# Optimization experiments

Hardware: AMD Instinct MI355X
Metric: run time of the kernel (lower is better)

Reference implementation:

```python
import jax, jax.numpy as jnp
import numpy as np

B, L, D, H = 4, 2048, 1024, 16
DK = D // H  # 64


def setup_inputs() -> dict:
    key = jax.random.key(0)
    ks = jax.random.split(key, 5)
    x = jax.random.normal(ks[0], (B, L, D), dtype=jnp.float32)
    scale = 1.0 / np.sqrt(D)
    W_qkv = jax.random.normal(ks[1], (D, 3 * D), dtype=jnp.float32) * scale
    b_qkv = jnp.zeros((3 * D,), dtype=jnp.float32)
    W_out = jax.random.normal(ks[2], (D, D), dtype=jnp.float32) * scale
    b_out = jnp.zeros((D,), dtype=jnp.float32)
    return {"x": x, "W_qkv": W_qkv, "b_qkv": b_qkv, "W_out": W_out, "b_out": b_out}


def reference(x, W_qkv, b_qkv, W_out, b_out):
    Bx, Lx, Dx = x.shape
    qkv = x @ W_qkv + b_qkv                      # [B, L, 3D]
    q, k, v = jnp.split(qkv, 3, axis=-1)
    # [B, H, L, d_k]
    q = q.reshape(Bx, Lx, H, DK).transpose(0, 2, 1, 3)
    k = k.reshape(Bx, Lx, H, DK).transpose(0, 2, 1, 3)
    v = v.reshape(Bx, Lx, H, DK).transpose(0, 2, 1, 3)
    scores = jnp.einsum('bhqd,bhkd->bhqk', q, k) / np.sqrt(DK)
    causal = jnp.tril(jnp.ones((Lx, Lx), dtype=bool))
    scores = jnp.where(causal[None, None], scores, -jnp.inf)
    attn = jax.nn.softmax(scores, axis=-1)       # [B, H, L, L]
    out = jnp.einsum('bhqk,bhkd->bhqd', attn, v)
    out = out.transpose(0, 2, 1, 3).reshape(Bx, Lx, Dx)
    return out @ W_out + b_out
```

## Files before the change

### kernel.cpp

```cpp
#include <hip/hip_runtime.h>
#include <stdint.h>

#define B_ 4
#define L_ 2048
#define D_ 1024
#define H_ 16
#define DK_ 64

typedef __attribute__((ext_vector_type(8))) short bf16x8;
typedef __attribute__((ext_vector_type(4))) float f32x4;
typedef unsigned short bfu;

#define MFMA(a, b, c) __builtin_amdgcn_mfma_f32_16x16x32_bf16((a), (b), (c), 0, 0, 0)

__device__ __forceinline__ unsigned short f2bf(float f) {
  union { float f; unsigned int u; } v; v.f = f;
  unsigned int u = v.u;
  return (unsigned short)((u + 0x7fffu + ((u >> 16) & 1u)) >> 16);
}

__device__ __forceinline__ void gll16(const void* g, void* l) {
  __builtin_amdgcn_global_load_lds(
      (const __attribute__((address_space(1))) void*)g,
      (__attribute__((address_space(3))) void*)l, 16, 0, 0);
}


__global__ __launch_bounds__(256) void cast_x(const float* __restrict__ in,
                                              bfu* __restrict__ out, int n4) {
  int i = blockIdx.x * 256 + threadIdx.x;
  if (i >= n4) return;
  float4 v = ((const float4*)in)[i];
  ushort4 o;
  o.x = f2bf(v.x); o.y = f2bf(v.y); o.z = f2bf(v.z); o.w = f2bf(v.w);
  ((ushort4*)out)[i] = o;
}

__global__ void transpose_cast(const float* __restrict__ in, bfu* __restrict__ out,
                               int R, int C) {
  __shared__ float tile[32][33];
  int c0 = blockIdx.x * 32, r0 = blockIdx.y * 32;
  int tx = threadIdx.x, ty = threadIdx.y;
#pragma unroll
  for (int i = ty; i < 32; i += 8)
    tile[i][tx] = in[(size_t)(r0 + i) * C + c0 + tx];
  __syncthreads();
#pragma unroll
  for (int i = ty; i < 32; i += 8)
    out[(size_t)(c0 + i) * R + r0 + tx] = f2bf(tile[tx][i]);
}


template <int EPI>
__global__ __launch_bounds__(256, 3) void gemm_bt(
    const bfu* __restrict__ A, const bfu* __restrict__ Bt,
    const float* __restrict__ bias, bfu* __restrict__ Qg, bfu* __restrict__ Kg,
    bfu* __restrict__ Vtg, float* __restrict__ Out, int M, int N, int K) {
  __shared__ __align__(16) bfu As[128 * 64];
  __shared__ __align__(16) bfu Bs[128 * 64];
  const int tid = threadIdx.x;
  const int lane = tid & 63;
  const int w = tid >> 6;
  const int wr = w >> 1, wc = w & 1;
  const int m0 = blockIdx.y * 128;
  const int n0 = blockIdx.x * 128;
  const int l15 = lane & 15, l4 = lane >> 4;

  f32x4 acc[4][4] = {};

  for (int k0 = 0; k0 < K; k0 += 64) {
    __syncthreads();
#pragma unroll
    for (int i = 0; i < 4; ++i) {
      int lb = i * 256 + tid;
      int r = lb >> 3;
      int c16p = lb & 7;
      int c16 = c16p ^ (r & 7);
      gll16(A + (size_t)(m0 + r) * K + k0 + c16 * 8, (char*)As + (size_t)lb * 16);
      gll16(Bt + (size_t)(n0 + r) * K + k0 + c16 * 8, (char*)Bs + (size_t)lb * 16);
    }
    __syncthreads();
#pragma unroll
    for (int kk = 0; kk < 2; ++kk) {
      bf16x8 af[4], bfr[4];
#pragma unroll
      for (int mi = 0; mi < 4; ++mi) {
        int r = wr * 64 + mi * 16 + l15;
        int c16 = (kk * 4 + l4) ^ (r & 7);
        af[mi] = *(const bf16x8*)((const char*)As + (size_t)r * 128 + c16 * 16);
      }
#pragma unroll
      for (int ni = 0; ni < 4; ++ni) {
        int r = wc * 64 + ni * 16 + l15;
        int c16 = (kk * 4 + l4) ^ (r & 7);
        bfr[ni] = *(const bf16x8*)((const char*)Bs + (size_t)r * 128 + c16 * 16);
      }
#pragma unroll
      for (int mi = 0; mi < 4; ++mi)
#pragma unroll
        for (int ni = 0; ni < 4; ++ni)
          acc[mi][ni] = MFMA(af[mi], bfr[ni], acc[mi][ni]);
    }
  }

#pragma unroll
  for (int ni = 0; ni < 4; ++ni) {
    int gn = n0 + wc * 64 + ni * 16 + l15;
    float bv = bias[gn];
    if (EPI == 0) {
      int sec = gn >> 10;
      int rem = gn & 1023;
      int hh = rem >> 6, dk = rem & 63;
#pragma unroll
      for (int mi = 0; mi < 4; ++mi) {
#pragma unroll
        for (int rg = 0; rg < 4; ++rg) {
          int gm = m0 + wr * 64 + mi * 16 + l4 * 4 + rg;
          int bb = gm >> 11, ll = gm & 2047;
          float v = acc[mi][ni][rg] + bv;
          size_t hd = (size_t)(bb * H_ + hh);
          if (sec == 0)
            Qg[(hd * L_ + ll) * DK_ + dk] = f2bf(v * 0.18033688011112042f);
          else if (sec == 1)
            Kg[(hd * L_ + ll) * DK_ + dk] = f2bf(v);
          else {
            int kv = ll & 63;
            int s = (kv & 32) | (((kv >> 2) & 3) << 3) | (((kv >> 4) & 1) << 2) | (kv & 3);
            Vtg[(hd * DK_ + dk) * L_ + ((ll & ~63) | s)] = f2bf(v);
          }
        }
      }
    } else {
#pragma unroll
      for (int mi = 0; mi < 4; ++mi)
#pragma unroll
        for (int rg = 0; rg < 4; ++rg) {
          int gm = m0 + wr * 64 + mi * 16 + l4 * 4 + rg;
          Out[(size_t)gm * 1024 + gn] = acc[mi][ni][rg] + bv;
        }
    }
  }
}


__global__ __launch_bounds__(256, 4) void attn(const bfu* __restrict__ Qg,
                                               const bfu* __restrict__ Kg,
                                               const bfu* __restrict__ Vtg,
                                               bfu* __restrict__ Ao) {
  __shared__ __align__(16) bfu Ks[2 * 64 * 64];
  __shared__ __align__(16) bfu Vs[2 * 64 * 64];
  __shared__ __align__(16) bfu Qs[64 * 64];

  const int tid = threadIdx.x;
  const int lane = tid & 63;
  const int w = tid >> 6;
  const int l15 = lane & 15, l4 = lane >> 4;

  const int hid = blockIdx.x;
  const int xcd = hid & 7, slot = hid >> 3;
  const int bh = (xcd << 3) | (slot >> 4);
  const int xq = slot & 15;
  const int b = bh >> 4, h = bh & 15;

  for (int seg = 0; seg < 2; ++seg) {
    const int qb = (seg == 0) ? xq : 31 - xq;
    const int q0 = qb * 64;
    const int nt = qb + 1;

#pragma unroll
    for (int i = 0; i < 2; ++i) {
      int lb = i * 256 + tid;
      int r = lb >> 3, c16 = (lb & 7) ^ (r & 7);
      gll16(Qg + ((size_t)bh * L_ + q0 + r) * DK_ + c16 * 8, (char*)Qs + lb * 16);
      gll16(Kg + ((size_t)bh * L_ + r) * DK_ + c16 * 8, (char*)Ks + lb * 16);
      gll16(Vtg + ((size_t)bh * DK_ + r) * L_ + c16 * 8, (char*)Vs + lb * 16);
    }
    asm volatile("s_waitcnt vmcnt(0)" ::: "memory");
    asm volatile("s_barrier" ::: "memory");

    bf16x8 qf[2];
#pragma unroll
    for (int kk = 0; kk < 2; ++kk) {
      int r = w * 16 + l15;
      int c16 = (kk * 4 + l4) ^ (r & 7);
      qf[kk] = *(const bf16x8*)((const char*)Qs + r * 128 + c16 * 16);
    }

    f32x4 acco[4] = {};
    float m = -1e30f, l = 0.f;

    for (int t = 0; t < nt; ++t) {
      const int cur = t & 1;
      const char* Kc = (const char*)Ks + cur * 8192;
      const char* Vc = (const char*)Vs + cur * 8192;

      if (t + 1 < nt) {
        const int nb = (t + 1) & 1, nkv = (t + 1) * 64;
#pragma unroll
        for (int i = 0; i < 2; ++i) {
          int lb = i * 256 + tid;
          int r = lb >> 3, c16 = (lb & 7) ^ (r & 7);
          gll16(Kg + ((size_t)bh * L_ + nkv + r) * DK_ + c16 * 8,
                (char*)Ks + nb * 8192 + lb * 16);
          gll16(Vtg + ((size_t)bh * DK_ + r) * L_ + nkv + c16 * 8,
                (char*)Vs + nb * 8192 + lb * 16);
        }
        asm volatile("s_waitcnt vmcnt(4)" ::: "memory");
      } else {
        asm volatile("s_waitcnt vmcnt(0)" ::: "memory");
      }
      asm volatile("s_barrier" ::: "memory");

      f32x4 s[4] = {};
      __builtin_amdgcn_s_setprio(1);
#pragma unroll
      for (int kk = 0; kk < 2; ++kk)
#pragma unroll
        for (int ni = 0; ni < 4; ++ni) {
          int r = ni * 16 + l15;
          int c16 = (kk * 4 + l4) ^ (r & 7);
          bf16x8 kf = *(const bf16x8*)(Kc + r * 128 + c16 * 16);
          s[ni] = MFMA(kf, qf[kk], s[ni]);
        }
      __builtin_amdgcn_s_setprio(0);

      if (t == nt - 1) {
        int ql = w * 16 + l15;
#pragma unroll
        for (int ni = 0; ni < 4; ++ni) {
          int kvl = ni * 16 + l4 * 4;
#pragma unroll
          for (int rg = 0; rg < 4; ++rg)
            if (kvl + rg > ql) s[ni][rg] = -1e30f;
        }
      }

      float mx = fmaxf(fmaxf(fmaxf(s[0][0], s[0][1]), fmaxf(s[0][2], s[0][3])),
                       fmaxf(fmaxf(s[1][0], s[1][1]), fmaxf(s[1][2], s[1][3])));
      mx = fmaxf(mx, fmaxf(fmaxf(fmaxf(s[2][0], s[2][1]), fmaxf(s[2][2], s[2][3])),
                           fmaxf(fmaxf(s[3][0], s[3][1]), fmaxf(s[3][2], s[3][3]))));
      mx = fmaxf(mx, __shfl_xor(mx, 16));
      mx = fmaxf(mx, __shfl_xor(mx, 32));
      if (__any(mx - m > 11.0f)) {
        float mn = fmaxf(m, mx);
        float sc = __builtin_amdgcn_exp2f(m - mn);
        m = mn;
        l *= sc;
#pragma unroll
        for (int rg = 0; rg < 4; ++rg) {
          float scq = __shfl(sc, l4 * 4 + rg);
          acco[0][rg] *= scq; acco[1][rg] *= scq;
          acco[2][rg] *= scq; acco[3][rg] *= scq;
        }
      }

      uint32_t pk[4][2];
#pragma unroll
      for (int ni = 0; ni < 4; ++ni) {
        float p0 = __builtin_amdgcn_exp2f(s[ni][0] - m);
        float p1 = __builtin_amdgcn_exp2f(s[ni][1] - m);
        float p2 = __builtin_amdgcn_exp2f(s[ni][2] - m);
        float p3 = __builtin_amdgcn_exp2f(s[ni][3] - m);
        l += (p0 + p1) + (p2 + p3);
        asm("v_cvt_pk_bf16_f32 %0, %1, %2" : "=v"(pk[ni][0]) : "v"(p0), "v"(p1));
        asm("v_cvt_pk_bf16_f32 %0, %1, %2" : "=v"(pk[ni][1]) : "v"(p2), "v"(p3));
      }

      __builtin_amdgcn_s_setprio(1);
#pragma unroll
      for (int kk = 0; kk < 2; ++kk) {
        union { uint32_t wd[4]; bf16x8 v; } u;
        u.wd[0] = pk[2 * kk][0];
        u.wd[1] = pk[2 * kk][1];
        u.wd[2] = pk[2 * kk + 1][0];
        u.wd[3] = pk[2 * kk + 1][1];
#pragma unroll
        for (int ni = 0; ni < 4; ++ni) {
          int r = ni * 16 + l15;
          int c16 = (kk * 4 + l4) ^ (r & 7);
          bf16x8 vf = *(const bf16x8*)(Vc + r * 128 + c16 * 16);
          acco[ni] = MFMA(u.v, vf, acco[ni]);
        }
      }
      __builtin_amdgcn_s_setprio(0);

      asm volatile("s_barrier" ::: "memory");
    }

    float ls = l;
    ls += __shfl_xor(ls, 16);
    ls += __shfl_xor(ls, 32);
    float linv = 1.0f / ls;
#pragma unroll
    for (int rg = 0; rg < 4; ++rg) {
      float lq = __shfl(linv, l4 * 4 + rg);
      int q = q0 + w * 16 + l4 * 4 + rg;
#pragma unroll
      for (int ni = 0; ni < 4; ++ni) {
        int d = ni * 16 + l15;
        Ao[((size_t)b * L_ + q) * D_ + h * DK_ + d] = f2bf(acco[ni][rg] * lq);
      }
    }
  }
}


extern "C" void kernel_launch(void* const* d_in, const int* in_sizes, int n_in,
                              void* d_out, int out_size, void* d_ws, size_t ws_size,
                              hipStream_t stream) {
  const float* x = (const float*)d_in[0];
  const float* W_qkv = (const float*)d_in[1];
  const float* b_qkv = (const float*)d_in[2];
  const float* W_out = (const float*)d_in[3];
  const float* b_out = (const float*)d_in[4];
  float* out = (float*)d_out;

  char* ws = (char*)d_ws;
  bfu* xb     = (bfu*)(ws);
  bfu* Wqkv_t = (bfu*)(ws + 16777216);
  bfu* Wout_t = (bfu*)(ws + 23068672);
  bfu* Qg     = (bfu*)(ws + 25165824);
  bfu* Kg     = (bfu*)(ws + 41943040);
  bfu* Vtg    = (bfu*)(ws + 58720256);
  bfu* Ao     = (bfu*)(ws + 75497472);

  cast_x<<<8192, 256, 0, stream>>>(x, xb, 2097152);
  transpose_cast<<<dim3(96, 32), dim3(32, 8), 0, stream>>>(W_qkv, Wqkv_t, 1024, 3072);
  transpose_cast<<<dim3(32, 32), dim3(32, 8), 0, stream>>>(W_out, Wout_t, 1024, 1024);

  gemm_bt<0><<<dim3(24, 64), 256, 0, stream>>>(xb, Wqkv_t, b_qkv, Qg, Kg, Vtg,
                                               nullptr, 8192, 3072, 1024);
  attn<<<1024, 256, 0, stream>>>(Qg, Kg, Vtg, Ao);
  gemm_bt<1><<<dim3(8, 64), 256, 0, stream>>>(Ao, Wout_t, b_out, nullptr, nullptr,
                                              nullptr, out, 8192, 1024, 1024);
}
```

Before: 184.5 us.

## Replace GEMM with 256x256 8-wave double-buffered pipelined kernel

Replaces the 128x128 single-buffered GEMM with a 256x256-tile, 512-thread kernel. It double-buffers LDS, interleaves global-to-LDS staging of the next K tile with MFMA work in four quarter-phases, and raises MFMA wave priority. It also adds an XCD-aware block swizzle and, for the V section, stages the transposed output through LDS so Vt rows are written as coalesced 16-byte stores. This aims to hide load latency and raise data reuse, at the cost of 128 KB of LDS, more accumulator registers, lower occupancy, and fewer blocks (128 for the output GEMM).

```diff
diff --git a/kernel.cpp b/kernel.cpp
--- a/kernel.cpp
+++ b/kernel.cpp
@@ -52,94 +52,196 @@
 
 
 template <int EPI>
-__global__ __launch_bounds__(256, 3) void gemm_bt(
+__global__ __launch_bounds__(512, 2) void gemm8(
     const bfu* __restrict__ A, const bfu* __restrict__ Bt,
     const float* __restrict__ bias, bfu* __restrict__ Qg, bfu* __restrict__ Kg,
     bfu* __restrict__ Vtg, float* __restrict__ Out, int M, int N, int K) {
-  __shared__ __align__(16) bfu As[128 * 64];
-  __shared__ __align__(16) bfu Bs[128 * 64];
+  __shared__ __align__(16) bfu LDSb[65536];
   const int tid = threadIdx.x;
   const int lane = tid & 63;
   const int w = tid >> 6;
-  const int wr = w >> 1, wc = w & 1;
-  const int m0 = blockIdx.y * 128;
-  const int n0 = blockIdx.x * 128;
+  const int wm = w >> 2, wn = w & 3;
   const int l15 = lane & 15, l4 = lane >> 4;
 
-  f32x4 acc[4][4] = {};
-
-  for (int k0 = 0; k0 < K; k0 += 64) {
-    __syncthreads();
-#pragma unroll
-    for (int i = 0; i < 4; ++i) {
-      int lb = i * 256 + tid;
-      int r = lb >> 3;
-      int c16p = lb & 7;
-      int c16 = c16p ^ (r & 7);
-      gll16(A + (size_t)(m0 + r) * K + k0 + c16 * 8, (char*)As + (size_t)lb * 16);
-      gll16(Bt + (size_t)(n0 + r) * K + k0 + c16 * 8, (char*)Bs + (size_t)lb * 16);
-    }
-    __syncthreads();
-#pragma unroll
-    for (int kk = 0; kk < 2; ++kk) {
-      bf16x8 af[4], bfr[4];
-#pragma unroll
-      for (int mi = 0; mi < 4; ++mi) {
-        int r = wr * 64 + mi * 16 + l15;
-        int c16 = (kk * 4 + l4) ^ (r & 7);
-        af[mi] = *(const bf16x8*)((const char*)As + (size_t)r * 128 + c16 * 16);
-      }
+  const int nwg = gridDim.x;
+  const int cpx = nwg >> 3;
+  const int bid = (int)blockIdx.x;
+  const int swz = (bid & 7) * cpx + (bid >> 3);
+  const int m0 = (swz & 31) * 256;
+  const int n0 = (swz >> 5) * 256;
+
+#define STAGE(t_, ev_)                                                        \
+  {                                                                           \
+    const int c_ = (t_) & 1;                                                  \
+    bfu* lb_ = ((ev_) == 0 || (ev_) == 3) ? (LDSb + c_ * 16384)               \
+                                          : (LDSb + 32768 + c_ * 16384);      \
+    const bfu* gs_ = ((ev_) == 0 || (ev_) == 3) ? A : Bt;                     \
+    const int g0_ = ((ev_) == 0 || (ev_) == 3) ? m0 : n0;                     \
+    _Pragma("unroll") for (int j_ = 0; j_ < 2; ++j_) {                        \
+      int idx_ = j_ * 512 + tid;                                              \
+      int r7_ = idx_ >> 3;                                                    \
+      int row_;                                                               \
+      if ((ev_) == 0) row_ = r7_ + ((r7_ >> 6) << 6);                         \
+      else if ((ev_) == 3) row_ = 64 + r7_ + ((r7_ >> 6) << 6);               \
+      else if ((ev_) == 1) row_ = r7_ + ((r7_ >> 5) << 5);                    \
+      else row_ = 32 + r7_ + ((r7_ >> 5) << 5);                               \
+      int c16_ = (idx_ & 7) ^ (row_ & 7);                                     \
+      gll16(gs_ + (size_t)(g0_ + row_) * K + (t_) * 64 + c16_ * 8,            \
+            (char*)lb_ + row_ * 128 + (idx_ & 7) * 16);                       \
+    }                                                                         \
+  }
+
+#define VMCNT(n_) asm volatile("s_waitcnt vmcnt(" #n_ ")" ::: "memory")
+#define BARRIER() asm volatile("s_barrier" ::: "memory")
+
+  f32x4 acc[8][4] = {};
+  bf16x8 af[4][2], bfA[2][2], bfB[2][2];
+
+  auto lda = [&](int c, int half) {
+    const char* base = (const char*)(LDSb + c * 16384);
+#pragma unroll
+    for (int mi = 0; mi < 4; ++mi)
+#pragma unroll
+      for (int kk = 0; kk < 2; ++kk) {
+        int row = wm * 128 + half * 64 + mi * 16 + l15;
+        int ch = (kk * 4 + l4) ^ (row & 7);
+        af[mi][kk] = *(const bf16x8*)(base + row * 128 + ch * 16);
+      }
+  };
+  auto ldb = [&](int c, int half, bf16x8 (*dst)[2]) {
+    const char* base = (const char*)(LDSb + 32768 + c * 16384);
+#pragma unroll
+    for (int ni = 0; ni < 2; ++ni)
+#pragma unroll
+      for (int kk = 0; kk < 2; ++kk) {
+        int row = wn * 64 + half * 32 + ni * 16 + l15;
+        int ch = (kk * 4 + l4) ^ (row & 7);
+        dst[ni][kk] = *(const bf16x8*)(base + row * 128 + ch * 16);
+      }
+  };
+
+#define MM(mo_, no_, bfX_)                                                    \
+  __builtin_amdgcn_s_setprio(1);                                              \
+  _Pragma("unroll") for (int mi_ = 0; mi_ < 4; ++mi_)                         \
+  _Pragma("unroll") for (int ni_ = 0; ni_ < 2; ++ni_)                         \
+  _Pragma("unroll") for (int kk_ = 0; kk_ < 2; ++kk_)                         \
+    acc[(mo_) + mi_][(no_) + ni_] =                                           \
+        MFMA(af[mi_][kk_], bfX_[ni_][kk_], acc[(mo_) + mi_][(no_) + ni_]);    \
+  __builtin_amdgcn_s_setprio(0);
+
+  STAGE(0, 0); STAGE(0, 1); STAGE(0, 2); STAGE(0, 3);
+  VMCNT(4);
+  BARRIER();
+
+  const int NT = K >> 6;
+  for (int t = 0; t < NT - 1; ++t) {
+    const int c = t & 1, tn = t + 1;
+    lda(c, 0); ldb(c, 0, bfA);
+    STAGE(tn, 0);
+    MM(0, 0, bfA);
+    VMCNT(4); BARRIER();
+    ldb(c, 1, bfB);
+    STAGE(tn, 1);
+    MM(0, 2, bfB);
+    VMCNT(4); BARRIER();
+    lda(c, 1);
+    STAGE(tn, 2);
+    MM(4, 2, bfB);
+    BARRIER();
+    STAGE(tn, 3);
+    MM(4, 0, bfA);
+    VMCNT(4); BARRIER();
+  }
+  {
+    const int c = (NT - 1) & 1;
+    lda(c, 0); ldb(c, 0, bfA);
+    MM(0, 0, bfA);
+    VMCNT(2); BARRIER();
+    ldb(c, 1, bfB);
+    MM(0, 2, bfB);
+    VMCNT(0); BARRIER();
+    lda(c, 1);
+    MM(4, 2, bfB);
+    MM(4, 0, bfA);
+  }
+
+  if (EPI == 1) {
+#pragma unroll
+    for (int ni = 0; ni < 4; ++ni) {
+      int gn = n0 + wn * 64 + ni * 16 + l15;
+      float bv = bias[gn];
+#pragma unroll
+      for (int mi = 0; mi < 8; ++mi)
+#pragma unroll
+        for (int rg = 0; rg < 4; ++rg) {
+          int gm = m0 + wm * 128 + mi * 16 + l4 * 4 + rg;
+          Out[(size_t)gm * N + gn] = acc[mi][ni][rg] + bv;
+        }
+    }
+  } else {
+    const int sec = n0 >> 10;
+    if (sec < 2) {
+      bfu* dst = (sec == 0) ? Qg : Kg;
+      const float scale = (sec == 0) ? 0.18033688011112042f : 1.0f;
 #pragma unroll
       for (int ni = 0; ni < 4; ++ni) {
-        int r = wc * 64 + ni * 16 + l15;
-        int c16 = (kk * 4 + l4) ^ (r & 7);
-        bfr[ni] = *(const bf16x8*)((const char*)Bs + (size_t)r * 128 + c16 * 16);
-      }
-#pragma unroll
-      for (int mi = 0; mi < 4; ++mi)
-#pragma unroll
-        for (int ni = 0; ni < 4; ++ni)
-          acc[mi][ni] = MFMA(af[mi], bfr[ni], acc[mi][ni]);
+        int gn = n0 + wn * 64 + ni * 16 + l15;
+        int rem = gn & 1023;
+        int hh = rem >> 6, dk = rem & 63;
+        float bv = bias[gn];
+#pragma unroll
+        for (int mi = 0; mi < 8; ++mi)
+#pragma unroll
+          for (int rg = 0; rg < 4; ++rg) {
+            int gm = m0 + wm * 128 + mi * 16 + l4 * 4 + rg;
+            int bb = gm >> 11, ll = gm & 2047;
+            dst[(((size_t)(bb * H_ + hh)) * L_ + ll) * DK_ + dk] =
+                f2bf((acc[mi][ni][rg] + bv) * scale);
+          }
+      }
+    } else {
+      __syncthreads();
+#pragma unroll
+      for (int ni = 0; ni < 4; ++ni) {
+        int n_local = wn * 64 + ni * 16 + l15;
+        int gn = n0 + n_local;
+        float bv = bias[gn];
+        int swzn = (n_local & 7) << 4;
+#pragma unroll
+        for (int mi = 0; mi < 8; ++mi) {
+          int m_base = wm * 128 + mi * 16 + l4 * 4;
+          int k6 = m_base & 63;
+          int p0 = (m_base & ~63) |
+                   ((k6 & 32) | (((k6 >> 2) & 3) << 3) | (((k6 >> 4) & 1) << 2));
+          float v0 = acc[mi][ni][0] + bv, v1 = acc[mi][ni][1] + bv;
+          float v2 = acc[mi][ni][2] + bv, v3 = acc[mi][ni][3] + bv;
+          uint32_t w01, w23;
+          asm("v_cvt_pk_bf16_f32 %0, %1, %2" : "=v"(w01) : "v"(v0), "v"(v1));
+          asm("v_cvt_pk_bf16_f32 %0, %1, %2" : "=v"(w23) : "v"(v2), "v"(v3));
+          *(uint32_t*)((char*)LDSb + n_local * 512 + ((2 * p0) ^ swzn)) = w01;
+          *(uint32_t*)((char*)LDSb + n_local * 512 + ((2 * p0 + 4) ^ swzn)) = w23;
+        }
+      }
+      __syncthreads();
+      int n = tid >> 1;
+      int cb = (tid & 1) * 16;
+      int gnn = n0 + n;
+      int hh = (gnn >> 6) & 15, dk = gnn & 63;
+      size_t rowbase =
+          (((size_t)((m0 >> 11) * H_ + hh)) * DK_ + dk) * L_ + (m0 & 2047);
+#pragma unroll
+      for (int j = 0; j < 16; ++j) {
+        int ch = cb + j;
+        bf16x8 vv = *(const bf16x8*)((char*)LDSb + n * 512 +
+                                     ((ch * 16) ^ ((n & 7) << 4)));
+        *(bf16x8*)(Vtg + rowbase + ch * 8) = vv;
+      }
     }
   }
-
-#pragma unroll
-  for (int ni = 0; ni < 4; ++ni) {
-    int gn = n0 + wc * 64 + ni * 16 + l15;
-    float bv = bias[gn];
-    if (EPI == 0) {
-      int sec = gn >> 10;
-      int rem = gn & 1023;
-      int hh = rem >> 6, dk = rem & 63;
-#pragma unroll
-      for (int mi = 0; mi < 4; ++mi) {
-#pragma unroll
-        for (int rg = 0; rg < 4; ++rg) {
-          int gm = m0 + wr * 64 + mi * 16 + l4 * 4 + rg;
-          int bb = gm >> 11, ll = gm & 2047;
-          float v = acc[mi][ni][rg] + bv;
-          size_t hd = (size_t)(bb * H_ + hh);
-          if (sec == 0)
-            Qg[(hd * L_ + ll) * DK_ + dk] = f2bf(v * 0.18033688011112042f);
-          else if (sec == 1)
-            Kg[(hd * L_ + ll) * DK_ + dk] = f2bf(v);
-          else {
-            int kv = ll & 63;
-            int s = (kv & 32) | (((kv >> 2) & 3) << 3) | (((kv >> 4) & 1) << 2) | (kv & 3);
-            Vtg[(hd * DK_ + dk) * L_ + ((ll & ~63) | s)] = f2bf(v);
-          }
-        }
-      }
-    } else {
-#pragma unroll
-      for (int mi = 0; mi < 4; ++mi)
-#pragma unroll
-        for (int rg = 0; rg < 4; ++rg) {
-          int gm = m0 + wr * 64 + mi * 16 + l4 * 4 + rg;
-          Out[(size_t)gm * 1024 + gn] = acc[mi][ni][rg] + bv;
-        }
-    }
-  }
+#undef STAGE
+#undef VMCNT
+#undef BARRIER
+#undef MM
 }
 
 
@@ -328,9 +430,9 @@
   transpose_cast<<<dim3(96, 32), dim3(32, 8), 0, stream>>>(W_qkv, Wqkv_t, 1024, 3072);
   transpose_cast<<<dim3(32, 32), dim3(32, 8), 0, stream>>>(W_out, Wout_t, 1024, 1024);
 
-  gemm_bt<0><<<dim3(24, 64), 256, 0, stream>>>(xb, Wqkv_t, b_qkv, Qg, Kg, Vtg,
-                                               nullptr, 8192, 3072, 1024);
+  gemm8<0><<<384, 512, 0, stream>>>(xb, Wqkv_t, b_qkv, Qg, Kg, Vtg, nullptr,
+                                    8192, 3072, 1024);
   attn<<<1024, 256, 0, stream>>>(Qg, Kg, Vtg, Ao);
-  gemm_bt<1><<<dim3(8, 64), 256, 0, stream>>>(Ao, Wout_t, b_out, nullptr, nullptr,
-                                              nullptr, out, 8192, 1024, 1024);
-}
+  gemm8<1><<<128, 512, 0, stream>>>(Ao, Wout_t, b_out, nullptr, nullptr, nullptr,
+                                    out, 8192, 1024, 1024);
+}
```

Result: no change. 181.7 us (-1.5%).
